# Performance work log

Hardware: AMD Instinct MI355X
Metric: run time of the kernel (lower is better)

The kernel has to match this reference:

```python
import jax, jax.numpy as jnp
import numpy as np

B, F, N, D = 4, 5, 2048, 256


def setup_inputs() -> dict:
    key = jax.random.key(0)
    k1, k2 = jax.random.split(key)
    x = jax.random.normal(k1, (B, F, N, D), dtype=jnp.float32)
    y = jax.random.normal(k2, (B, F, N, D), dtype=jnp.float32)
    return {"x": x, "y": y}


def _weight(a, b):
    # pairwise_distance with p=2 in the original is sum((a-b)**2)**(1/(2-1)),
    # i.e. SQUARED euclidean distance (no sqrt). Use gram expansion to avoid
    # materializing the [B,F,N,N,D] difference tensor.
    a2 = jnp.sum(a * a, axis=-1)                      # [B,F,N]
    b2 = jnp.sum(b * b, axis=-1)                      # [B,F,M]
    ab = jnp.einsum('bfnd,bfmd->bfnm', a, b)          # [B,F,N,M]
    d = a2[..., :, None] + b2[..., None, :] - 2.0 * ab  # squared dists
    # min over neighbors (dim=1 of the per-frame matrix), mean over query
    # nodes, then mean over frames -> one scalar per batch element.
    return jnp.mean(jnp.min(d, axis=-1), axis=(-1, -2))  # [B]


def _normalize(f):
    # min/max over the node dim (dim=2), per (batch, frame, feature)
    mn = jnp.min(f, axis=2, keepdims=True)
    mx = jnp.max(f, axis=2, keepdims=True)
    return (f - mn) / (mx - mn)


def reference(x, y):
    wx = 1.0 / (1.0 + _weight(x, y))  # [B]
    wy = 1.0 / (1.0 + _weight(y, x))  # [B]
    nx = _normalize(x)
    ny = _normalize(y)
    return wx[:, None, None, None] * nx + wy[:, None, None, None] * ny
```

## Files before the change

kernel.cpp:

```cpp
#include <hip/hip_runtime.h>

typedef unsigned int u32;
typedef unsigned short u16;
typedef __attribute__((ext_vector_type(8))) short short8;
typedef __attribute__((ext_vector_type(4))) float floatx4;

#define NB 4
#define NF 5
#define NN 2048
#define NDM 256
#define NBF (NB*NF)
#define NBFN (NBF*NN)
#define NBFD (NBF*NDM)

#define AS1 __attribute__((address_space(1)))
#define AS3 __attribute__((address_space(3)))

__device__ u16    g_xb[(size_t)NBF*NN*NDM];
__device__ u16    g_yb[(size_t)NBF*NN*NDM];
__device__ float  g_a2[NBFN];
__device__ float  g_b2[NBFN];
__device__ float  g_rpart[(size_t)8*NBFN];
__device__ float  g_cpart[(size_t)32*NBFN];
__device__ float  g_pmn[2][(size_t)32*NBFD];
__device__ float  g_pmx[2][(size_t)32*NBFD];
__device__ float  g_bfsum[2*NBF];
__device__ float4 g_coef[NBFD];

__device__ __forceinline__ u16 cvt_bf16(float f){
  u32 b = __float_as_uint(f);
  return (u16)((b + 0x7FFFu + ((b >> 16) & 1u)) >> 16);
}
__device__ __forceinline__ void load16(const void* g, void* l){
  __builtin_amdgcn_global_load_lds((AS1 const void*)g, (AS3 void*)l, 16, 0, 0);
}

__global__ void __launch_bounds__(256) k_prep(const float* __restrict__ x,
                                              const float* __restrict__ y){
  int bi = blockIdx.x;
  int tensor = bi >= (NBF*32); int rem = bi - tensor*(NBF*32);
  int bf = rem >> 5; int chunk = rem & 31;
  size_t rbase = (size_t)bf*NN + (size_t)chunk*64;
  const float* src = (tensor ? y : x) + rbase*NDM;
  u16*  dst  = (tensor ? g_yb : g_xb) + rbase*NDM;
  float* sums = (tensor ? g_b2 : g_a2) + bf*NN + chunk*64;
  int w = threadIdx.x >> 6, l = threadIdx.x & 63;

  float4 vmn = make_float4(INFINITY,INFINITY,INFINITY,INFINITY);
  float4 vmx = make_float4(-INFINITY,-INFINITY,-INFINITY,-INFINITY);
  for (int i = 0; i < 16; ++i){
    int row = w + 4*i;
    float4 v = ((const float4*)(src + (size_t)row*NDM))[l];
    float s = v.x*v.x + v.y*v.y + v.z*v.z + v.w*v.w;
    #pragma unroll
    for (int m = 1; m < 64; m <<= 1) s += __shfl_xor(s, m, 64);
    ((ushort4*)(dst + (size_t)row*NDM))[l] =
        make_ushort4(cvt_bf16(v.x), cvt_bf16(v.y), cvt_bf16(v.z), cvt_bf16(v.w));
    if (l == 0) sums[row] = s;
    vmn.x = fminf(vmn.x, v.x); vmn.y = fminf(vmn.y, v.y);
    vmn.z = fminf(vmn.z, v.z); vmn.w = fminf(vmn.w, v.w);
    vmx.x = fmaxf(vmx.x, v.x); vmx.y = fmaxf(vmx.y, v.y);
    vmx.z = fmaxf(vmx.z, v.z); vmx.w = fmaxf(vmx.w, v.w);
  }
  __shared__ float4 smn[4][64], smx[4][64];
  smn[w][l] = vmn; smx[w][l] = vmx;
  __syncthreads();
  if (w == 0){
    float4 a = smn[0][l], b_ = smn[1][l], c = smn[2][l], d = smn[3][l];
    float4 e = smx[0][l], f = smx[1][l], g = smx[2][l], h = smx[3][l];
    float4 mn4 = make_float4(fminf(fminf(a.x,b_.x), fminf(c.x,d.x)),
                             fminf(fminf(a.y,b_.y), fminf(c.y,d.y)),
                             fminf(fminf(a.z,b_.z), fminf(c.z,d.z)),
                             fminf(fminf(a.w,b_.w), fminf(c.w,d.w)));
    float4 mx4 = make_float4(fmaxf(fmaxf(e.x,f.x), fmaxf(g.x,h.x)),
                             fmaxf(fmaxf(e.y,f.y), fmaxf(g.y,h.y)),
                             fmaxf(fmaxf(e.z,f.z), fmaxf(g.z,h.z)),
                             fmaxf(fmaxf(e.w,f.w), fmaxf(g.w,h.w)));
    ((float4*)&g_pmn[tensor][(size_t)chunk*NBFD + bf*NDM])[l] = mn4;
    ((float4*)&g_pmx[tensor][(size_t)chunk*NBFD + bf*NDM])[l] = mx4;
  }
}

__global__ void __launch_bounds__(256) k_gemm(){
  __shared__ u16 As[128*64];
  __shared__ u16 Bs[128*64];
  const int bf = blockIdx.z;
  const int i0 = blockIdx.y * 128;
  const int jq = blockIdx.x;
  const int t = threadIdx.x;
  const int w = t >> 6, l = t & 63;
  const int wm = (w >> 1) * 64, wn = (w & 1) * 64;
  const int quad = l >> 4, c16 = l & 15;
  const u16* xb = g_xb + (size_t)bf * NN * NDM;
  const u16* yb = g_yb + (size_t)bf * NN * NDM;
  const int lr = l >> 3, gj = (l & 7) ^ lr;

  const float* a2 = g_a2 + bf*NN + i0;
  const float* b2 = g_b2 + bf*NN;
  float a2r[4][4];
  #pragma unroll
  for (int mb = 0; mb < 4; ++mb)
    #pragma unroll
    for (int r = 0; r < 4; ++r)
      a2r[mb][r] = a2[wm + mb*16 + quad*4 + r];

  float rm[4][4];
  #pragma unroll
  for (int mb = 0; mb < 4; ++mb)
    #pragma unroll
    for (int r = 0; r < 4; ++r) rm[mb][r] = INFINITY;

  for (int jj = 0; jj < 4; ++jj){
    const int j0 = jq*512 + jj*128;
    floatx4 acc[4][4] = {};
    for (int kc = 0; kc < 4; ++kc){
      const int k0 = kc * 64;
      __syncthreads();
      #pragma unroll
      for (int q = 0; q < 4; ++q){
        const int c = w*4 + q;
        const int r = c*8 + lr;
        load16(xb + (size_t)(i0 + r)*NDM + k0 + gj*8, &As[c*512]);
        load16(yb + (size_t)(j0 + r)*NDM + k0 + gj*8, &Bs[c*512]);
      }
      __syncthreads();
      #pragma unroll
      for (int kb = 0; kb < 2; ++kb){
        const int p8 = ((kb*4 + quad) ^ (c16 & 7)) * 8;
        short8 af[4], bq[4];
        #pragma unroll
        for (int mb = 0; mb < 4; ++mb)
          af[mb] = *(const short8*)&As[(wm + mb*16 + c16)*64 + p8];
        #pragma unroll
        for (int nb = 0; nb < 4; ++nb)
          bq[nb] = *(const short8*)&Bs[(wn + nb*16 + c16)*64 + p8];
        #pragma unroll
        for (int mb = 0; mb < 4; ++mb)
          #pragma unroll
          for (int nb = 0; nb < 4; ++nb)
            acc[mb][nb] = __builtin_amdgcn_mfma_f32_16x16x32_bf16(af[mb], bq[nb], acc[mb][nb], 0, 0, 0);
      }
    }
    float bcol[4], colm[4];
    #pragma unroll
    for (int nb = 0; nb < 4; ++nb){
      bcol[nb] = b2[j0 + wn + nb*16 + c16];
      colm[nb] = INFINITY;
    }
    #pragma unroll
    for (int mb = 0; mb < 4; ++mb)
      #pragma unroll
      for (int r = 0; r < 4; ++r)
        #pragma unroll
        for (int nb = 0; nb < 4; ++nb){
          float dd = a2r[mb][r] + bcol[nb] - 2.0f * acc[mb][nb][r];
          rm[mb][r] = fminf(rm[mb][r], dd);
          colm[nb] = fminf(colm[nb], dd);
        }
    #pragma unroll
    for (int nb = 0; nb < 4; ++nb){
      float cm = colm[nb];
      cm = fminf(cm, __shfl_xor(cm, 16, 64));
      cm = fminf(cm, __shfl_xor(cm, 32, 64));
      if (quad == 0)
        g_cpart[(size_t)(blockIdx.y*2 + (w>>1))*NBFN + bf*NN + j0 + wn + nb*16 + c16] = cm;
    }
  }
  #pragma unroll
  for (int mb = 0; mb < 4; ++mb)
    #pragma unroll
    for (int r = 0; r < 4; ++r){
      float v = rm[mb][r];
      v = fminf(v, __shfl_xor(v, 1, 64));
      v = fminf(v, __shfl_xor(v, 2, 64));
      v = fminf(v, __shfl_xor(v, 4, 64));
      v = fminf(v, __shfl_xor(v, 8, 64));
      if (c16 == 0)
        g_rpart[(size_t)(jq*2 + (w&1))*NBFN + bf*NN + i0 + wm + mb*16 + quad*4 + r] = v;
    }
}

__global__ void __launch_bounds__(256) k_weight(){
  int bf = blockIdx.x;
  float srow = 0.f, scol = 0.f;
  for (int i = threadIdx.x; i < NN; i += 256){
    size_t base = (size_t)bf*NN + i;
    float m = INFINITY, c = INFINITY;
    #pragma unroll
    for (int p = 0; p < 8; ++p)  m = fminf(m, g_rpart[(size_t)p*NBFN + base]);
    #pragma unroll
    for (int p = 0; p < 32; ++p) c = fminf(c, g_cpart[(size_t)p*NBFN + base]);
    srow += m; scol += c;
  }
  #pragma unroll
  for (int m = 1; m < 64; m <<= 1){
    srow += __shfl_xor(srow, m, 64);
    scol += __shfl_xor(scol, m, 64);
  }
  __shared__ float pr[4], pcn[4];
  int w = threadIdx.x >> 6, l = threadIdx.x & 63;
  if (l == 0){ pr[w] = srow; pcn[w] = scol; }
  __syncthreads();
  if (threadIdx.x == 0){
    g_bfsum[bf]       = pr[0]+pr[1]+pr[2]+pr[3];
    g_bfsum[NBF + bf] = pcn[0]+pcn[1]+pcn[2]+pcn[3];
  }
}

__global__ void k_coef(){
  int idx = blockIdx.x * 256 + threadIdx.x;
  int bf = idx >> 8;
  int b = bf / NF;
  float swx = 0.f, swy = 0.f;
  #pragma unroll
  for (int f = 0; f < NF; ++f){
    swx += g_bfsum[b*NF + f];
    swy += g_bfsum[NBF + b*NF + f];
  }
  float wx = 1.0f / (1.0f + swx * (1.0f/(NF*NN)));
  float wy = 1.0f / (1.0f + swy * (1.0f/(NF*NN)));
  float mnx = INFINITY, mxx = -INFINITY, mny = INFINITY, mxy = -INFINITY;
  #pragma unroll
  for (int c = 0; c < 32; ++c){
    mnx = fminf(mnx, g_pmn[0][(size_t)c*NBFD + idx]);
    mxx = fmaxf(mxx, g_pmx[0][(size_t)c*NBFD + idx]);
    mny = fminf(mny, g_pmn[1][(size_t)c*NBFD + idx]);
    mxy = fmaxf(mxy, g_pmx[1][(size_t)c*NBFD + idx]);
  }
  float sx = wx / (mxx - mnx), sy = wy / (mxy - mny);
  g_coef[idx] = make_float4(sx, -sx * mnx, sy, -sy * mny);
}

__global__ void __launch_bounds__(256) k_out(const float4* __restrict__ x,
                                             const float4* __restrict__ y,
                                             float4* __restrict__ out){
  size_t i = (size_t)blockIdx.x * 256 + threadIdx.x;
  float4 xv = x[i], yv = y[i];
  size_t base = i * 4;
  int bf = (int)(base >> 19);
  int d0 = (int)(base & 255);
  const float4* cf = &g_coef[bf * 256 + d0];
  float4 c0 = cf[0], c1 = cf[1], c2 = cf[2], c3 = cf[3];
  float4 o;
  o.x = c0.x * xv.x + c0.y + c0.z * yv.x + c0.w;
  o.y = c1.x * xv.y + c1.y + c1.z * yv.y + c1.w;
  o.z = c2.x * xv.z + c2.y + c2.z * yv.z + c2.w;
  o.w = c3.x * xv.w + c3.y + c3.z * yv.w + c3.w;
  out[i] = o;
}

extern "C" void kernel_launch(void* const* d_in, const int* in_sizes, int n_in,
                              void* d_out, int out_size, void* d_ws, size_t ws_size,
                              hipStream_t stream) {
  const float* x = (const float*)d_in[0];
  const float* y = (const float*)d_in[1];
  (void)d_ws; (void)ws_size; (void)in_sizes; (void)n_in; (void)out_size;

  k_prep  <<<dim3(1280),       dim3(256), 0, stream>>>(x, y);
  k_gemm  <<<dim3(4, 16, 20),  dim3(256), 0, stream>>>();
  k_weight<<<dim3(20),         dim3(256), 0, stream>>>();
  k_coef  <<<dim3(20),         dim3(256), 0, stream>>>();
  k_out   <<<dim3(10240),      dim3(256), 0, stream>>>((const float4*)x, (const float4*)y,
                                                       (float4*)d_out);
}
```

Baseline: 238.5 us.

## Keep A tile in registers, widen warp N-tile, parallelize weight reduction, nontemporal output

The GEMM kernel now loads each warp's 32 rows of x directly into registers for the full K range and drops the shared A tile. Only the y tile is staged through LDS, and each warp covers all 128 columns, so the partial-min layouts change to 4 row partials and 64 column partials. The weight reduction is split across 160 blocks that combine their sums with atomics into a buffer zeroed in k_prep. The output kernel uses nontemporal stores. The register-resident A operand raises register pressure (launch bounds of 256,2), and the larger column-partial buffer adds reduction traffic.

```diff
diff --git a/kernel.cpp b/kernel.cpp
--- a/kernel.cpp
+++ b/kernel.cpp
@@ -20,8 +20,8 @@
 __device__ u16    g_yb[(size_t)NBF*NN*NDM];
 __device__ float  g_a2[NBFN];
 __device__ float  g_b2[NBFN];
-__device__ float  g_rpart[(size_t)8*NBFN];
-__device__ float  g_cpart[(size_t)32*NBFN];
+__device__ float  g_rpart[(size_t)4*NBFN];
+__device__ float  g_cpart[(size_t)64*NBFN];
 __device__ float  g_pmn[2][(size_t)32*NBFD];
 __device__ float  g_pmx[2][(size_t)32*NBFD];
 __device__ float  g_bfsum[2*NBF];
@@ -38,6 +38,7 @@
 __global__ void __launch_bounds__(256) k_prep(const float* __restrict__ x,
                                               const float* __restrict__ y){
   int bi = blockIdx.x;
+  if (bi == 0 && threadIdx.x < 2*NBF) g_bfsum[threadIdx.x] = 0.f;
   int tensor = bi >= (NBF*32); int rem = bi - tensor*(NBF*32);
   int bf = rem >> 5; int chunk = rem & 31;
   size_t rbase = (size_t)bf*NN + (size_t)chunk*64;
@@ -81,93 +82,96 @@
   }
 }
 
-__global__ void __launch_bounds__(256) k_gemm(){
-  __shared__ u16 As[128*64];
+__global__ void __launch_bounds__(256, 2) k_gemm(){
   __shared__ u16 Bs[128*64];
   const int bf = blockIdx.z;
   const int i0 = blockIdx.y * 128;
   const int jq = blockIdx.x;
   const int t = threadIdx.x;
   const int w = t >> 6, l = t & 63;
-  const int wm = (w >> 1) * 64, wn = (w & 1) * 64;
   const int quad = l >> 4, c16 = l & 15;
+  const int wrow = w * 32;
   const u16* xb = g_xb + (size_t)bf * NN * NDM;
   const u16* yb = g_yb + (size_t)bf * NN * NDM;
   const int lr = l >> 3, gj = (l & 7) ^ lr;
 
-  const float* a2 = g_a2 + bf*NN + i0;
+  short8 af[2][8];
+  #pragma unroll
+  for (int mb = 0; mb < 2; ++mb){
+    const u16* rp = xb + (size_t)(i0 + wrow + mb*16 + c16) * NDM + quad*8;
+    #pragma unroll
+    for (int ks = 0; ks < 8; ++ks)
+      af[mb][ks] = *(const short8*)(rp + ks*32);
+  }
+  const float* a2 = g_a2 + bf*NN + i0 + wrow;
   const float* b2 = g_b2 + bf*NN;
-  float a2r[4][4];
-  #pragma unroll
-  for (int mb = 0; mb < 4; ++mb)
+  float a2r[2][4];
+  #pragma unroll
+  for (int mb = 0; mb < 2; ++mb)
     #pragma unroll
     for (int r = 0; r < 4; ++r)
-      a2r[mb][r] = a2[wm + mb*16 + quad*4 + r];
-
-  float rm[4][4];
-  #pragma unroll
-  for (int mb = 0; mb < 4; ++mb)
+      a2r[mb][r] = a2[mb*16 + quad*4 + r];
+
+  float rm[2][4];
+  #pragma unroll
+  for (int mb = 0; mb < 2; ++mb)
     #pragma unroll
     for (int r = 0; r < 4; ++r) rm[mb][r] = INFINITY;
 
   for (int jj = 0; jj < 4; ++jj){
     const int j0 = jq*512 + jj*128;
-    floatx4 acc[4][4] = {};
+    floatx4 acc[2][8] = {};
+    #pragma unroll
     for (int kc = 0; kc < 4; ++kc){
-      const int k0 = kc * 64;
       __syncthreads();
       #pragma unroll
       for (int q = 0; q < 4; ++q){
         const int c = w*4 + q;
         const int r = c*8 + lr;
-        load16(xb + (size_t)(i0 + r)*NDM + k0 + gj*8, &As[c*512]);
-        load16(yb + (size_t)(j0 + r)*NDM + k0 + gj*8, &Bs[c*512]);
+        load16(yb + (size_t)(j0 + r)*NDM + kc*64 + gj*8, &Bs[c*512]);
       }
       __syncthreads();
       #pragma unroll
       for (int kb = 0; kb < 2; ++kb){
         const int p8 = ((kb*4 + quad) ^ (c16 & 7)) * 8;
-        short8 af[4], bq[4];
+        short8 bq[8];
         #pragma unroll
-        for (int mb = 0; mb < 4; ++mb)
-          af[mb] = *(const short8*)&As[(wm + mb*16 + c16)*64 + p8];
+        for (int nb = 0; nb < 8; ++nb)
+          bq[nb] = *(const short8*)&Bs[(nb*16 + c16)*64 + p8];
         #pragma unroll
-        for (int nb = 0; nb < 4; ++nb)
-          bq[nb] = *(const short8*)&Bs[(wn + nb*16 + c16)*64 + p8];
-        #pragma unroll
-        for (int mb = 0; mb < 4; ++mb)
+        for (int mb = 0; mb < 2; ++mb)
           #pragma unroll
-          for (int nb = 0; nb < 4; ++nb)
-            acc[mb][nb] = __builtin_amdgcn_mfma_f32_16x16x32_bf16(af[mb], bq[nb], acc[mb][nb], 0, 0, 0);
+          for (int nb = 0; nb < 8; ++nb)
+            acc[mb][nb] = __builtin_amdgcn_mfma_f32_16x16x32_bf16(af[mb][kc*2+kb], bq[nb], acc[mb][nb], 0, 0, 0);
       }
     }
-    float bcol[4], colm[4];
-    #pragma unroll
-    for (int nb = 0; nb < 4; ++nb){
-      bcol[nb] = b2[j0 + wn + nb*16 + c16];
+    float bcol[8], colm[8];
+    #pragma unroll
+    for (int nb = 0; nb < 8; ++nb){
+      bcol[nb] = b2[j0 + nb*16 + c16];
       colm[nb] = INFINITY;
     }
     #pragma unroll
-    for (int mb = 0; mb < 4; ++mb)
+    for (int mb = 0; mb < 2; ++mb)
       #pragma unroll
       for (int r = 0; r < 4; ++r)
         #pragma unroll
-        for (int nb = 0; nb < 4; ++nb){
+        for (int nb = 0; nb < 8; ++nb){
           float dd = a2r[mb][r] + bcol[nb] - 2.0f * acc[mb][nb][r];
           rm[mb][r] = fminf(rm[mb][r], dd);
           colm[nb] = fminf(colm[nb], dd);
         }
     #pragma unroll
-    for (int nb = 0; nb < 4; ++nb){
+    for (int nb = 0; nb < 8; ++nb){
       float cm = colm[nb];
       cm = fminf(cm, __shfl_xor(cm, 16, 64));
       cm = fminf(cm, __shfl_xor(cm, 32, 64));
       if (quad == 0)
-        g_cpart[(size_t)(blockIdx.y*2 + (w>>1))*NBFN + bf*NN + j0 + wn + nb*16 + c16] = cm;
-    }
-  }
-  #pragma unroll
-  for (int mb = 0; mb < 4; ++mb)
+        g_cpart[(size_t)(blockIdx.y*4 + w)*NBFN + bf*NN + j0 + nb*16 + c16] = cm;
+    }
+  }
+  #pragma unroll
+  for (int mb = 0; mb < 2; ++mb)
     #pragma unroll
     for (int r = 0; r < 4; ++r){
       float v = rm[mb][r];
@@ -176,34 +180,33 @@
       v = fminf(v, __shfl_xor(v, 4, 64));
       v = fminf(v, __shfl_xor(v, 8, 64));
       if (c16 == 0)
-        g_rpart[(size_t)(jq*2 + (w&1))*NBFN + bf*NN + i0 + wm + mb*16 + quad*4 + r] = v;
+        g_rpart[(size_t)jq*NBFN + bf*NN + i0 + wrow + mb*16 + quad*4 + r] = v;
     }
 }
 
 __global__ void __launch_bounds__(256) k_weight(){
-  int bf = blockIdx.x;
-  float srow = 0.f, scol = 0.f;
-  for (int i = threadIdx.x; i < NN; i += 256){
-    size_t base = (size_t)bf*NN + i;
-    float m = INFINITY, c = INFINITY;
-    #pragma unroll
-    for (int p = 0; p < 8; ++p)  m = fminf(m, g_rpart[(size_t)p*NBFN + base]);
-    #pragma unroll
-    for (int p = 0; p < 32; ++p) c = fminf(c, g_cpart[(size_t)p*NBFN + base]);
-    srow += m; scol += c;
-  }
-  #pragma unroll
-  for (int m = 1; m < 64; m <<= 1){
-    srow += __shfl_xor(srow, m, 64);
-    scol += __shfl_xor(scol, m, 64);
+  int bf = blockIdx.x >> 3;
+  int chunk = blockIdx.x & 7;
+  int i = chunk*256 + threadIdx.x;
+  size_t base = (size_t)bf*NN + i;
+  float m = INFINITY, c = INFINITY;
+  #pragma unroll
+  for (int p = 0; p < 4; ++p)  m = fminf(m, g_rpart[(size_t)p*NBFN + base]);
+  #pragma unroll
+  for (int p = 0; p < 64; ++p) c = fminf(c, g_cpart[(size_t)p*NBFN + base]);
+  float srow = m, scol = c;
+  #pragma unroll
+  for (int mm = 1; mm < 64; mm <<= 1){
+    srow += __shfl_xor(srow, mm, 64);
+    scol += __shfl_xor(scol, mm, 64);
   }
   __shared__ float pr[4], pcn[4];
   int w = threadIdx.x >> 6, l = threadIdx.x & 63;
   if (l == 0){ pr[w] = srow; pcn[w] = scol; }
   __syncthreads();
   if (threadIdx.x == 0){
-    g_bfsum[bf]       = pr[0]+pr[1]+pr[2]+pr[3];
-    g_bfsum[NBF + bf] = pcn[0]+pcn[1]+pcn[2]+pcn[3];
+    atomicAdd(&g_bfsum[bf],       pr[0]+pr[1]+pr[2]+pr[3]);
+    atomicAdd(&g_bfsum[NBF + bf], pcn[0]+pcn[1]+pcn[2]+pcn[3]);
   }
 }
 
@@ -233,7 +236,7 @@
 
 __global__ void __launch_bounds__(256) k_out(const float4* __restrict__ x,
                                              const float4* __restrict__ y,
-                                             float4* __restrict__ out){
+                                             floatx4* __restrict__ out){
   size_t i = (size_t)blockIdx.x * 256 + threadIdx.x;
   float4 xv = x[i], yv = y[i];
   size_t base = i * 4;
@@ -241,12 +244,12 @@
   int d0 = (int)(base & 255);
   const float4* cf = &g_coef[bf * 256 + d0];
   float4 c0 = cf[0], c1 = cf[1], c2 = cf[2], c3 = cf[3];
-  float4 o;
+  floatx4 o;
   o.x = c0.x * xv.x + c0.y + c0.z * yv.x + c0.w;
   o.y = c1.x * xv.y + c1.y + c1.z * yv.y + c1.w;
   o.z = c2.x * xv.z + c2.y + c2.z * yv.z + c2.w;
   o.w = c3.x * xv.w + c3.y + c3.z * yv.w + c3.w;
-  out[i] = o;
+  __builtin_nontemporal_store(o, &out[i]);
 }
 
 extern "C" void kernel_launch(void* const* d_in, const int* in_sizes, int n_in,
@@ -258,8 +261,8 @@
 
   k_prep  <<<dim3(1280),       dim3(256), 0, stream>>>(x, y);
   k_gemm  <<<dim3(4, 16, 20),  dim3(256), 0, stream>>>();
-  k_weight<<<dim3(20),         dim3(256), 0, stream>>>();
+  k_weight<<<dim3(160),        dim3(256), 0, stream>>>();
   k_coef  <<<dim3(20),         dim3(256), 0, stream>>>();
   k_out   <<<dim3(10240),      dim3(256), 0, stream>>>((const float4*)x, (const float4*)y,
-                                                       (float4*)d_out);
-}
+                                                       (floatx4*)d_out);
+}
```

New measurement: 228.4 us. 4.2% less time.
